# Optimization experiments

Measured on AMD Instinct MI355X. Metric: run time of the kernel, lower is better.

## Reference

```python
import jax, jax.numpy as jnp
import numpy as np

D_MODEL = 1024
N_HEADS = 16
HEAD_DIM = D_MODEL // N_HEADS


def setup_inputs() -> dict:
    key = jax.random.key(0)
    k1, k2, k3 = jax.random.split(key, 3)
    x = jax.random.normal(k1, (2, 2048, D_MODEL), dtype=jnp.float32)
    # nn.Linear weights: stored as [out, in]; y = x @ W.T
    W_qkv = jax.random.normal(k2, (3 * D_MODEL, D_MODEL), dtype=jnp.float32) * (1.0 / np.sqrt(D_MODEL))
    W_out = jax.random.normal(k3, (D_MODEL, D_MODEL), dtype=jnp.float32) * (1.0 / np.sqrt(D_MODEL))
    return {"x": x, "W_qkv": W_qkv, "W_out": W_out}


def reference(x, W_qkv, W_out):
    B, T, C = x.shape
    qkv = jnp.einsum('btc,oc->bto', x, W_qkv)  # [B,T,3C]
    q, k, v = jnp.split(qkv, 3, axis=-1)

    def split_heads(t):
        return t.reshape(B, T, N_HEADS, HEAD_DIM).transpose(0, 2, 1, 3)  # [B,H,T,D]

    q, k, v = split_heads(q), split_heads(k), split_heads(v)
    scale = jnp.asarray(1.0 / np.sqrt(HEAD_DIM), dtype=x.dtype)
    attn = jnp.einsum('bhqd,bhkd->bhqk', q, k) * scale  # [B,H,T,T]
    causal = jnp.tril(jnp.ones((T, T), dtype=bool))
    attn = jnp.where(causal, attn, -jnp.inf)
    attn = jax.nn.softmax(attn, axis=-1)
    out = jnp.einsum('bhqk,bhkd->bhqd', attn, v)
    out = out.transpose(0, 2, 1, 3).reshape(B, T, C)
    return jnp.einsum('btc,oc->bto', out, W_out)
```

## Files before the change

kernel.cpp:

```cpp
#include <hip/hip_runtime.h>

typedef float f32x4 __attribute__((ext_vector_type(4)));
typedef short short8 __attribute__((ext_vector_type(8)));

#define GBL(p) ((__attribute__((address_space(1))) void*)(p))
#define LDS(p) ((__attribute__((address_space(3))) void*)(p))

static __device__ __forceinline__ unsigned short f2bf(float x) {
  union { float f; unsigned u; } a; a.f = x;
  unsigned u = a.u;
  return (unsigned short)((u + 0x7FFFu + ((u >> 16) & 1u)) >> 16);
}

static __device__ __forceinline__ short8 ld8(const unsigned short* p) {
  return *(const short8*)(p);
}

static __device__ __forceinline__ f32x4 zero4() {
  f32x4 z = {0.f, 0.f, 0.f, 0.f};
  return z;
}

__global__ void cvt_kernel(const float4* __restrict__ in, ushort4* __restrict__ out, int n4) {
  int i = blockIdx.x * blockDim.x + threadIdx.x;
  if (i >= n4) return;
  float4 v = in[i];
  ushort4 o;
  o.x = f2bf(v.x); o.y = f2bf(v.y); o.z = f2bf(v.z); o.w = f2bf(v.w);
  out[i] = o;
}

template<int MODE>
__global__ __launch_bounds__(256) void gemm_bt(
    const unsigned short* __restrict__ A,
    const unsigned short* __restrict__ B,
    void* __restrict__ Cout, void* __restrict__ Cout2, void* __restrict__ Cout3,
    int M, int N, int K)
{
  __shared__ __align__(16) unsigned short As[128 * 32];
  __shared__ __align__(16) unsigned short Bs[128 * 32];

  const int t = threadIdx.x;
  const int lane = t & 63;
  const int w = t >> 6;
  const int wr = (w >> 1) * 64;
  const int wc = (w & 1) * 64;
  const int fr = lane & 15;
  const int kg = lane >> 4;
  const size_t rowBase = (size_t)blockIdx.y * 128;
  const size_t colBase = (size_t)blockIdx.x * 128;

  f32x4 acc[4][4];
  for (int m = 0; m < 4; ++m)
    for (int n = 0; n < 4; ++n) acc[m][n] = zero4();

  const unsigned short* ag = A + (rowBase + (t >> 2)) * (size_t)K + (t & 3) * 8;
  const unsigned short* bg = B + (colBase + (t >> 2)) * (size_t)K + (t & 3) * 8;
  unsigned short* asd = As + t * 8;
  unsigned short* bsd = Bs + t * 8;

  for (int k0 = 0; k0 < K; k0 += 32) {
    __builtin_amdgcn_global_load_lds(GBL(ag + k0),                   LDS(asd),        16, 0, 0);
    __builtin_amdgcn_global_load_lds(GBL(ag + (size_t)64 * K + k0),  LDS(asd + 2048), 16, 0, 0);
    __builtin_amdgcn_global_load_lds(GBL(bg + k0),                   LDS(bsd),        16, 0, 0);
    __builtin_amdgcn_global_load_lds(GBL(bg + (size_t)64 * K + k0),  LDS(bsd + 2048), 16, 0, 0);
    __syncthreads();
    short8 af[4], bf[4];
    for (int m = 0; m < 4; ++m) af[m] = ld8(As + (wr + m * 16 + fr) * 32 + kg * 8);
    for (int n = 0; n < 4; ++n) bf[n] = ld8(Bs + (wc + n * 16 + fr) * 32 + kg * 8);
    for (int m = 0; m < 4; ++m)
      for (int n = 0; n < 4; ++n)
        acc[m][n] = __builtin_amdgcn_mfma_f32_16x16x32_bf16(af[m], bf[n], acc[m][n], 0, 0, 0);
    __syncthreads();
  }

  for (int m = 0; m < 4; ++m)
    for (int n = 0; n < 4; ++n) {
      const size_t row = rowBase + wr + m * 16 + kg * 4;
      const size_t col = colBase + wc + n * 16 + fr;
      if (MODE == 0) {
        float* C = (float*)Cout;
        for (int j = 0; j < 4; ++j) C[(row + j) * N + col] = acc[m][n][j];
      } else {
        if (col < 1024) {
          unsigned short* Q = (unsigned short*)Cout;
          for (int j = 0; j < 4; ++j) Q[(row + j) * 1024 + col] = f2bf(acc[m][n][j]);
        } else if (col < 2048) {
          unsigned short* KF = (unsigned short*)Cout2;
          const int d_all = (int)col - 1024;
          const int hh = d_all >> 6, d = d_all & 63;
          const int c = d >> 5, kgp = (d >> 3) & 3, el = d & 7;
          for (int j = 0; j < 4; ++j) {
            const int r = (int)row + j;
            const int bp = r >> 11, s = r & 2047;
            const size_t addr =
                ((size_t)(((bp * 16 + hh) * 128 + (s >> 4)) * 2 + c)) * 512
                + (size_t)((kgp * 16 + (s & 15)) * 8 + el);
            KF[addr] = f2bf(acc[m][n][j]);
          }
        } else {
          unsigned short* VF = (unsigned short*)Cout3;
          const int d_all = (int)col - 2048;
          const int hh = d_all >> 6, dd = d_all & 63;
          const int nd = dd >> 4, frp = dd & 15;
          const int r0 = (int)row;
          const int bp = r0 >> 11, s = r0 & 2047;
          const size_t base =
              ((size_t)(((bp * 16 + hh) * 64 + (s >> 5)) * 4 + nd)) * 512
              + (size_t)((((s >> 3) & 3) * 16 + frp) * 8 + (s & 7));
          ushort4 o4;
          o4.x = f2bf(acc[m][n][0]); o4.y = f2bf(acc[m][n][1]);
          o4.z = f2bf(acc[m][n][2]); o4.w = f2bf(acc[m][n][3]);
          *(ushort4*)(VF + base) = o4;
        }
      }
    }
}

__global__ __launch_bounds__(256) void attn_kernel(
    const unsigned short* __restrict__ qb,
    const unsigned short* __restrict__ kfb,
    const unsigned short* __restrict__ vfb,
    unsigned short* __restrict__ om)
{
  __shared__ __align__(16) unsigned short Ps[4][16 * 32];

  const int bh = blockIdx.x;
  const int pr = blockIdx.y;
  const int b = bh >> 4, h = bh & 15;
  const int t = threadIdx.x;
  const int lane = t & 63, w = t >> 6;
  const int fr = lane & 15, kg = lane >> 4;
  const int lane8 = lane * 8;
  const size_t seq0 = (size_t)b * 2048;

  unsigned short* pw = &Ps[w][0];
  const float cs = 0.125f * 1.44269504f;
  const unsigned short* kfB = kfb + (size_t)bh * (128 * 2 * 512) + lane8;
  const unsigned short* vfB = vfb + (size_t)bh * (64 * 4 * 512) + lane8;
  const int rdswz = fr * 32 + (((kg ^ (fr >> 2)) & 3) << 3);

#define LOADKV(kr0, kf, vf) do {                                               \
    const unsigned short* kp = kfB + (size_t)((kr0) >> 4) * 1024;              \
    kf[0] = ld8(kp);        kf[1] = ld8(kp + 512);                             \
    kf[2] = ld8(kp + 1024); kf[3] = ld8(kp + 1536);                            \
    const unsigned short* vp = vfB + (size_t)((kr0) >> 5) * 2048;              \
    vf[0] = ld8(vp);        vf[1] = ld8(vp + 512);                             \
    vf[2] = ld8(vp + 1024); vf[3] = ld8(vp + 1536);                            \
  } while (0)

#define COMPUTE(kr0, kf, vf) do {                                              \
    f32x4 s0 = zero4(), s1 = zero4();                                          \
    __builtin_amdgcn_s_setprio(1);                                             \
    s0 = __builtin_amdgcn_mfma_f32_16x16x32_bf16(qf0, kf[0], s0, 0, 0, 0);     \
    s0 = __builtin_amdgcn_mfma_f32_16x16x32_bf16(qf1, kf[1], s0, 0, 0, 0);     \
    s1 = __builtin_amdgcn_mfma_f32_16x16x32_bf16(qf0, kf[2], s1, 0, 0, 0);     \
    s1 = __builtin_amdgcn_mfma_f32_16x16x32_bf16(qf1, kf[3], s1, 0, 0, 0);     \
    __builtin_amdgcn_s_setprio(0);                                             \
    _Pragma("unroll")                                                          \
    for (int j = 0; j < 4; ++j) {                                              \
      const int qrow = qrow0 + kg * 4 + j;                                     \
      const int r = kg * 4 + j;                                                \
      float a0 = ((kr0) + fr      <= qrow) ? s0[j] * cs : -1e30f;              \
      float a1 = ((kr0) + 16 + fr <= qrow) ? s1[j] * cs : -1e30f;              \
      float e0 = exp2f(a0);                                                    \
      float e1 = exp2f(a1);                                                    \
      l_run[j] += e0 + e1;                                                     \
      pw[r * 32 + ((((fr >> 3)       ^ kg) & 3) << 3) + (fr & 7)] = f2bf(e0);  \
      pw[r * 32 + (((2 + (fr >> 3))  ^ kg) * 8 & 31) + (fr & 7)] = f2bf(e1);   \
    }                                                                          \
    short8 pf = ld8(pw + rdswz);                                               \
    __builtin_amdgcn_s_setprio(1);                                             \
    _Pragma("unroll")                                                          \
    for (int nd = 0; nd < 4; ++nd)                                             \
      o[nd] = __builtin_amdgcn_mfma_f32_16x16x32_bf16(pf, vf[nd], o[nd], 0, 0, 0); \
    __builtin_amdgcn_s_setprio(0);                                             \
  } while (0)

  for (int half = 0; half < 2; ++half) {
    const int qt = half ? (31 - pr) : pr;
    const int qrow0 = qt * 64 + w * 16;
    const int lastkt = (qrow0 + 15) >> 5;

    const unsigned short* qp = qb + (seq0 + qrow0 + fr) * 1024 + h * 64;
    const short8 qf0 = ld8(qp + kg * 8);
    const short8 qf1 = ld8(qp + 32 + kg * 8);

    float l_run[4] = {0.f, 0.f, 0.f, 0.f};
    f32x4 o[4];
    for (int n = 0; n < 4; ++n) o[n] = zero4();

    short8 kA[4], vA[4], kB[4], vB[4];
    LOADKV(0, kA, vA);
    int kt = 0;
    while (true) {
      int nkr = (kt < lastkt) ? (kt + 1) * 32 : 0;
      LOADKV(nkr, kB, vB);
      COMPUTE(kt * 32, kA, vA);
      ++kt; if (kt > lastkt) break;
      nkr = (kt < lastkt) ? (kt + 1) * 32 : 0;
      LOADKV(nkr, kA, vA);
      COMPUTE(kt * 32, kB, vB);
      ++kt; if (kt > lastkt) break;
    }

    for (int j = 0; j < 4; ++j) {
      float l = l_run[j];
      l += __shfl_xor(l, 1);
      l += __shfl_xor(l, 2);
      l += __shfl_xor(l, 4);
      l += __shfl_xor(l, 8);
      const float inv = 1.0f / l;
      for (int nd = 0; nd < 4; ++nd) {
        om[(seq0 + qrow0 + kg * 4 + j) * 1024 + h * 64 + nd * 16 + fr] =
            f2bf(o[nd][j] * inv);
      }
    }
  }
#undef LOADKV
#undef COMPUTE
}

extern "C" void kernel_launch(void* const* d_in, const int* in_sizes, int n_in,
                              void* d_out, int out_size, void* d_ws, size_t ws_size,
                              hipStream_t stream) {
  const float* x    = (const float*)d_in[0];
  const float* Wqkv = (const float*)d_in[1];
  const float* Wout = (const float*)d_in[2];
  float* out = (float*)d_out;

  char* ws = (char*)d_ws;
  unsigned short* xb    = (unsigned short*)(ws);
  unsigned short* wqkvb = (unsigned short*)(ws + 8388608);
  unsigned short* woutb = (unsigned short*)(ws + 14680064);
  unsigned short* qbuf  = (unsigned short*)(ws + 16777216);
  unsigned short* kfb   = (unsigned short*)(ws + 25165824);
  unsigned short* vfb   = (unsigned short*)(ws + 33554432);
  unsigned short* attno = (unsigned short*)(ws + 41943040);

  cvt_kernel<<<dim3(4096), dim3(256), 0, stream>>>((const float4*)x,    (ushort4*)xb,    1048576);
  cvt_kernel<<<dim3(3072), dim3(256), 0, stream>>>((const float4*)Wqkv, (ushort4*)wqkvb, 786432);
  cvt_kernel<<<dim3(1024), dim3(256), 0, stream>>>((const float4*)Wout, (ushort4*)woutb, 262144);

  gemm_bt<1><<<dim3(24, 32), dim3(256), 0, stream>>>(xb, wqkvb, (void*)qbuf, (void*)kfb, (void*)vfb, 4096, 3072, 1024);

  attn_kernel<<<dim3(32, 16), dim3(256), 0, stream>>>(qbuf, kfb, vfb, attno);

  gemm_bt<0><<<dim3(8, 32), dim3(256), 0, stream>>>(attno, woutb, (void*)out, nullptr, nullptr, 4096, 1024, 1024);
}
```

Measured before the change: 199.7 us.

## Software-pipeline attention PV with next QK, fold scale into Q, skip masks

Folds the softmax scale and log2(e) into the Q projection epilogue, so the attention inner loop no longer multiplies each score. The K and V loads are split, and the loop is restructured so the PV MFMA for the previous tile runs after the QK and softmax of the current tile, hiding the LDS write/read latency of the P tile. The causal mask is applied only on the diagonal tile, and the LDS write addresses are precomputed once. The cost is more live registers (two V buffers plus pf) and more intricate loop control, which could lower occupancy.

```diff
diff --git a/kernel.cpp b/kernel.cpp
--- a/kernel.cpp
+++ b/kernel.cpp
@@ -84,7 +84,8 @@
       } else {
         if (col < 1024) {
           unsigned short* Q = (unsigned short*)Cout;
-          for (int j = 0; j < 4; ++j) Q[(row + j) * 1024 + col] = f2bf(acc[m][n][j]);
+          for (int j = 0; j < 4; ++j)
+            Q[(row + j) * 1024 + col] = f2bf(acc[m][n][j] * 0.18033688f);
         } else if (col < 2048) {
           unsigned short* KF = (unsigned short*)Cout2;
           const int d_all = (int)col - 1024;
@@ -135,21 +136,32 @@
   const size_t seq0 = (size_t)b * 2048;
 
   unsigned short* pw = &Ps[w][0];
-  const float cs = 0.125f * 1.44269504f;
   const unsigned short* kfB = kfb + (size_t)bh * (128 * 2 * 512) + lane8;
   const unsigned short* vfB = vfb + (size_t)bh * (64 * 4 * 512) + lane8;
+
+  unsigned short* pws0[4];
+  unsigned short* pws1[4];
+#pragma unroll
+  for (int j = 0; j < 4; ++j) {
+    const int r = kg * 4 + j;
+    pws0[j] = pw + r * 32 + ((((fr >> 3)     ^ kg) & 3) << 3) + (fr & 7);
+    pws1[j] = pw + r * 32 + ((((2 + (fr >> 3)) ^ kg) & 3) << 3) + (fr & 7);
+  }
   const int rdswz = fr * 32 + (((kg ^ (fr >> 2)) & 3) << 3);
 
-#define LOADKV(kr0, kf, vf) do {                                               \
+#define LOADK(kr0, kf) do {                                                    \
     const unsigned short* kp = kfB + (size_t)((kr0) >> 4) * 1024;              \
     kf[0] = ld8(kp);        kf[1] = ld8(kp + 512);                             \
     kf[2] = ld8(kp + 1024); kf[3] = ld8(kp + 1536);                            \
+  } while (0)
+
+#define LOADV(kr0, vf) do {                                                    \
     const unsigned short* vp = vfB + (size_t)((kr0) >> 5) * 2048;              \
     vf[0] = ld8(vp);        vf[1] = ld8(vp + 512);                             \
     vf[2] = ld8(vp + 1024); vf[3] = ld8(vp + 1536);                            \
   } while (0)
 
-#define COMPUTE(kr0, kf, vf) do {                                              \
+#define QKSM(kr0, kf, DOMASK) do {                                             \
     f32x4 s0 = zero4(), s1 = zero4();                                          \
     __builtin_amdgcn_s_setprio(1);                                             \
     s0 = __builtin_amdgcn_mfma_f32_16x16x32_bf16(qf0, kf[0], s0, 0, 0, 0);     \
@@ -159,17 +171,22 @@
     __builtin_amdgcn_s_setprio(0);                                             \
     _Pragma("unroll")                                                          \
     for (int j = 0; j < 4; ++j) {                                              \
-      const int qrow = qrow0 + kg * 4 + j;                                     \
-      const int r = kg * 4 + j;                                                \
-      float a0 = ((kr0) + fr      <= qrow) ? s0[j] * cs : -1e30f;              \
-      float a1 = ((kr0) + 16 + fr <= qrow) ? s1[j] * cs : -1e30f;              \
-      float e0 = exp2f(a0);                                                    \
-      float e1 = exp2f(a1);                                                    \
+      float a0 = s0[j];                                                        \
+      float a1 = s1[j];                                                        \
+      if (DOMASK) {                                                            \
+        const int qrow = qrow0 + kg * 4 + j;                                   \
+        a0 = ((kr0) + fr      <= qrow) ? a0 : -1e30f;                          \
+        a1 = ((kr0) + 16 + fr <= qrow) ? a1 : -1e30f;                          \
+      }                                                                        \
+      const float e0 = exp2f(a0);                                              \
+      const float e1 = exp2f(a1);                                              \
       l_run[j] += e0 + e1;                                                     \
-      pw[r * 32 + ((((fr >> 3)       ^ kg) & 3) << 3) + (fr & 7)] = f2bf(e0);  \
-      pw[r * 32 + (((2 + (fr >> 3))  ^ kg) * 8 & 31) + (fr & 7)] = f2bf(e1);   \
+      *pws0[j] = f2bf(e0);                                                     \
+      *pws1[j] = f2bf(e1);                                                     \
     }                                                                          \
-    short8 pf = ld8(pw + rdswz);                                               \
+  } while (0)
+
+#define PV(vf) do {                                                            \
     __builtin_amdgcn_s_setprio(1);                                             \
     _Pragma("unroll")                                                          \
     for (int nd = 0; nd < 4; ++nd)                                             \
@@ -177,10 +194,12 @@
     __builtin_amdgcn_s_setprio(0);                                             \
   } while (0)
 
+#define READP do { pf = ld8(pw + rdswz); } while (0)
+
   for (int half = 0; half < 2; ++half) {
     const int qt = half ? (31 - pr) : pr;
     const int qrow0 = qt * 64 + w * 16;
-    const int lastkt = (qrow0 + 15) >> 5;
+    const int nfull = qrow0 >> 5;
 
     const unsigned short* qp = qb + (seq0 + qrow0 + fr) * 1024 + h * 64;
     const short8 qf0 = ld8(qp + kg * 8);
@@ -190,18 +209,30 @@
     f32x4 o[4];
     for (int n = 0; n < 4; ++n) o[n] = zero4();
 
-    short8 kA[4], vA[4], kB[4], vB[4];
-    LOADKV(0, kA, vA);
+    short8 kA[4], kB[4], vA[4], vB[4], pf;
+    LOADK(0, kA);
     int kt = 0;
     while (true) {
-      int nkr = (kt < lastkt) ? (kt + 1) * 32 : 0;
-      LOADKV(nkr, kB, vB);
-      COMPUTE(kt * 32, kA, vA);
-      ++kt; if (kt > lastkt) break;
-      nkr = (kt < lastkt) ? (kt + 1) * 32 : 0;
-      LOADKV(nkr, kA, vA);
-      COMPUTE(kt * 32, kB, vB);
-      ++kt; if (kt > lastkt) break;
+      {
+        const int kn = (kt < nfull) ? (kt + 1) * 32 : nfull * 32;
+        LOADK(kn, kB);
+        LOADV(kt * 32, vA);
+        if (kt == nfull) { QKSM(kt * 32, kA, 1); } else { QKSM(kt * 32, kA, 0); }
+        if (kt > 0) PV(vB);
+        READP;
+      }
+      if (kt == nfull) { PV(vA); break; }
+      ++kt;
+      {
+        const int kn = (kt < nfull) ? (kt + 1) * 32 : nfull * 32;
+        LOADK(kn, kA);
+        LOADV(kt * 32, vB);
+        if (kt == nfull) { QKSM(kt * 32, kB, 1); } else { QKSM(kt * 32, kB, 0); }
+        PV(vA);
+        READP;
+      }
+      if (kt == nfull) { PV(vB); break; }
+      ++kt;
     }
 
     for (int j = 0; j < 4; ++j) {
@@ -217,8 +248,11 @@
       }
     }
   }
-#undef LOADKV
-#undef COMPUTE
+#undef LOADK
+#undef LOADV
+#undef QKSM
+#undef PV
+#undef READP
 }
 
 extern "C" void kernel_launch(void* const* d_in, const int* in_sizes, int n_in,
```

New measurement: 193.5 us. -3.1%, faster.
